# Kernel optimization log

Hardware: AMD Instinct MI355X
Metric: run time of the kernel (lower is better)

The kernel has to match this reference:

```python
import jax, jax.numpy as jnp
import numpy as np

GROUP_SIZE = 8
OUT_FEATURES = 4096
IN_FEATURES = 4096
G = OUT_FEATURES * IN_FEATURES // GROUP_SIZE  # number of quant groups


def setup_inputs() -> dict:
    key = jax.random.key(0)
    k1, k2, k3, k4, k5 = jax.random.split(key, 5)
    x = jax.random.normal(k1, (2, 2048, IN_FEATURES), dtype=jnp.float32)
    # packed uint8 bytes, stored as int32 for harness dtype support (values 0..255)
    weight_packed = jax.random.randint(k2, (G, GROUP_SIZE // 2), 0, 256, dtype=jnp.int32)
    weight_scale = jax.random.uniform(k3, (G, 1), dtype=jnp.float32)
    weight_bias = jax.random.normal(k4, (G, 1), dtype=jnp.float32)
    bias = jax.random.normal(k5, (OUT_FEATURES,), dtype=jnp.float32)
    return {"x": x, "weight_packed": weight_packed, "weight_scale": weight_scale,
            "weight_bias": weight_bias, "bias": bias}


def dequantize_4bit(packed, scale, wbias):
    # packed: [G, gs//2] ints in [0,256); each byte holds two 4-bit values
    low = (packed & 15).astype(jnp.float32)          # even positions
    high = ((packed >> 4) & 15).astype(jnp.float32)  # odd positions
    # interleave: q[:, ::2] = low, q[:, 1::2] = high
    q = jnp.stack([low, high], axis=-1).reshape(packed.shape[0], -1)  # [G, gs]
    return q * scale + wbias  # per-group scale and bias, broadcast [G,1]->[G,gs]


def reference(x, weight_packed, weight_scale, weight_bias, bias):
    w = dequantize_4bit(weight_packed, weight_scale, weight_bias)
    w = w.reshape(OUT_FEATURES, IN_FEATURES)
    # F.linear: y = x @ w.T + bias
    return jnp.einsum('bsi,oi->bso', x, w) + bias
```

## Files before the change

### kernel.cpp

```cpp
#include <hip/hip_runtime.h>
#include <hip/hip_bf16.h>
#include <stdint.h>

#define M_DIM 4096
#define N_DIM 4096
#define K_DIM 4096
#define NGROUPS (N_DIM * K_DIM / 8)

typedef __attribute__((ext_vector_type(4))) float f32x4;
typedef __attribute__((ext_vector_type(8))) short bf16x8;
typedef __attribute__((ext_vector_type(4))) int   i32x4;

__device__ __forceinline__ ushort f2bf(float f) {
  union { float f; uint32_t u; } v; v.f = f;
  uint32_t r = v.u + 0x7FFFu + ((v.u >> 16) & 1u);
  return (ushort)(r >> 16);
}

__global__ void k_dequant_w(const int* __restrict__ wp, const float* __restrict__ wsc,
                            const float* __restrict__ wbs, ushort* __restrict__ W) {
  const int g = blockIdx.x * 256 + threadIdx.x;
  i32x4 p = *(const i32x4*)(wp + (size_t)g * 4);
  const float s = wsc[g];
  const float b = wbs[g];
  bf16x8 o;
#pragma unroll
  for (int j = 0; j < 4; ++j) {
    const float lo = (float)(p[j] & 15)        * s + b;
    const float hi = (float)((p[j] >> 4) & 15) * s + b;
    o[2 * j]     = (short)f2bf(lo);
    o[2 * j + 1] = (short)f2bf(hi);
  }
  *(bf16x8*)(W + (size_t)g * 8) = o;
}

__global__ void k_cvt_x(const float* __restrict__ x, ushort* __restrict__ X) {
  const int t = blockIdx.x * 256 + threadIdx.x;
  f32x4 a = *(const f32x4*)(x + (size_t)t * 8);
  f32x4 b = *(const f32x4*)(x + (size_t)t * 8 + 4);
  bf16x8 o;
#pragma unroll
  for (int j = 0; j < 4; ++j) {
    o[j]     = (short)f2bf(a[j]);
    o[4 + j] = (short)f2bf(b[j]);
  }
  *(bf16x8*)(X + (size_t)t * 8) = o;
}


#define GLD(src, dst) __builtin_amdgcn_global_load_lds(                        \
    (const __attribute__((address_space(1))) void*)(src),                      \
    (__attribute__((address_space(3))) void*)(dst), 16, 0, 0)

__global__ __launch_bounds__(512, 2) void k_gemm_8ph(
    const ushort* __restrict__ A, const ushort* __restrict__ B,
    const float* __restrict__ bias, float* __restrict__ C) {
  __shared__ ushort sA[2][256 * 64];
  __shared__ ushort sB[2][256 * 64];
  const int tid  = threadIdx.x;
  const int lane = tid & 63;
  const int wid  = tid >> 6;
  const int wr   = wid >> 2;
  const int wc   = wid & 3;
  const int bm = blockIdx.x >> 4;
  const int bn = blockIdx.x & 15;

  const ushort* Ab = A + (size_t)bm * 256 * K_DIM;
  const ushort* Bb = B + (size_t)bn * 256 * K_DIM;

  const int srow = tid >> 3;
  const int scc  = (tid & 7) ^ ((tid >> 3) & 7);
  const int dofs = (tid >> 6) * 64 * 8;

  const int l15   = lane & 15;
  const int kx    = (lane >> 4) * 8;
  const int xsw   = (lane & 7) << 3;
  const int kidx0 = (0 * 32 + kx) ^ xsw;
  const int kidx1 = (1 * 32 + kx) ^ xsw;
  const int abase = (wr * 128 + l15) * 64;
  const int bbase = (wc * 64 + l15) * 64;

  f32x4 acc[8][4] = {};

#define STAGE_A(buf, kko)                                                      \
  _Pragma("unroll") for (int j = 0; j < 4; ++j)                                \
      GLD(Ab + (size_t)(j * 64 + srow) * K_DIM + (kko) + scc * 8,              \
          &sA[buf][j * 4096 + dofs]);
#define STAGE_B(buf, kko)                                                      \
  _Pragma("unroll") for (int j = 0; j < 4; ++j)                                \
      GLD(Bb + (size_t)(j * 64 + srow) * K_DIM + (kko) + scc * 8,              \
          &sB[buf][j * 4096 + dofs]);

  STAGE_A(0, 0);
  STAGE_B(0, 0);
  __syncthreads();

  bf16x8 af0[4][2], af1[4][2], bfA[2][2], bfB[2][2];
#pragma unroll
  for (int m = 0; m < 4; ++m) {
    af0[m][0] = *(const bf16x8*)(sA[0] + abase + m * 1024 + kidx0);
    af0[m][1] = *(const bf16x8*)(sA[0] + abase + m * 1024 + kidx1);
  }
#pragma unroll
  for (int n = 0; n < 2; ++n) {
    bfA[n][0] = *(const bf16x8*)(sB[0] + bbase + n * 1024 + kidx0);
    bfA[n][1] = *(const bf16x8*)(sB[0] + bbase + n * 1024 + kidx1);
  }

  for (int t = 0; t < 64; ++t) {
    const int b  = t & 1;
    const int kk = t * 64;
    const ushort* sAb = sA[b];
    const ushort* sBb = sB[b];
    const ushort* sAn = sA[b ^ 1];
    const ushort* sBn = sB[b ^ 1];

    if (t < 63) { STAGE_A(b ^ 1, kk + 64); }
#pragma unroll
    for (int n = 0; n < 2; ++n) {
      bfB[n][0] = *(const bf16x8*)(sBb + bbase + (2 + n) * 1024 + kidx0);
      bfB[n][1] = *(const bf16x8*)(sBb + bbase + (2 + n) * 1024 + kidx1);
    }
    __builtin_amdgcn_s_setprio(1);
#pragma unroll
    for (int m = 0; m < 4; ++m)
#pragma unroll
      for (int n = 0; n < 2; ++n)
#pragma unroll
        for (int kc = 0; kc < 2; ++kc)
          acc[m][n] = __builtin_amdgcn_mfma_f32_16x16x32_bf16(
              af0[m][kc], bfA[n][kc], acc[m][n], 0, 0, 0);
    __builtin_amdgcn_s_setprio(0);
    __builtin_amdgcn_s_barrier();

    if (t < 63) { STAGE_B(b ^ 1, kk + 64); }
#pragma unroll
    for (int m = 0; m < 4; ++m) {
      af1[m][0] = *(const bf16x8*)(sAb + abase + (4 + m) * 1024 + kidx0);
      af1[m][1] = *(const bf16x8*)(sAb + abase + (4 + m) * 1024 + kidx1);
    }
    __builtin_amdgcn_s_setprio(1);
#pragma unroll
    for (int m = 0; m < 4; ++m)
#pragma unroll
      for (int n = 0; n < 2; ++n)
#pragma unroll
        for (int kc = 0; kc < 2; ++kc)
          acc[m][2 + n] = __builtin_amdgcn_mfma_f32_16x16x32_bf16(
              af0[m][kc], bfB[n][kc], acc[m][2 + n], 0, 0, 0);
    __builtin_amdgcn_s_setprio(0);
    __builtin_amdgcn_s_barrier();

    __builtin_amdgcn_s_setprio(1);
#pragma unroll
    for (int m = 0; m < 4; ++m)
#pragma unroll
      for (int n = 0; n < 2; ++n)
#pragma unroll
        for (int kc = 0; kc < 2; ++kc)
          acc[4 + m][2 + n] = __builtin_amdgcn_mfma_f32_16x16x32_bf16(
              af1[m][kc], bfB[n][kc], acc[4 + m][2 + n], 0, 0, 0);
    __builtin_amdgcn_s_setprio(0);

    if (t < 63) { asm volatile("s_waitcnt vmcnt(0)" ::: "memory"); }
    __builtin_amdgcn_s_barrier();
    asm volatile("" ::: "memory");
    __builtin_amdgcn_s_setprio(1);
#pragma unroll
    for (int m = 0; m < 4; ++m)
#pragma unroll
      for (int n = 0; n < 2; ++n)
#pragma unroll
        for (int kc = 0; kc < 2; ++kc)
          acc[4 + m][n] = __builtin_amdgcn_mfma_f32_16x16x32_bf16(
              af1[m][kc], bfA[n][kc], acc[4 + m][n], 0, 0, 0);
    __builtin_amdgcn_s_setprio(0);
    if (t < 63) {
#pragma unroll
      for (int m = 0; m < 4; ++m) {
        af0[m][0] = *(const bf16x8*)(sAn + abase + m * 1024 + kidx0);
        af0[m][1] = *(const bf16x8*)(sAn + abase + m * 1024 + kidx1);
      }
#pragma unroll
      for (int n = 0; n < 2; ++n) {
        bfA[n][0] = *(const bf16x8*)(sBn + bbase + n * 1024 + kidx0);
        bfA[n][1] = *(const bf16x8*)(sBn + bbase + n * 1024 + kidx1);
      }
    }
  }

  const int fr = lane & 15;
  const int fq = lane >> 4;
  const int growbase = bm * 256 + wr * 128;
  const int gcolbase = bn * 256 + wc * 64;
#pragma unroll
  for (int ni = 0; ni < 4; ++ni) {
    const int col = gcolbase + ni * 16 + fr;
    const float bv = bias[col];
#pragma unroll
    for (int mi = 0; mi < 8; ++mi) {
      float* cp = C + (size_t)(growbase + mi * 16 + fq * 4) * N_DIM + col;
#pragma unroll
      for (int r = 0; r < 4; ++r)
        cp[(size_t)r * N_DIM] = acc[mi][ni][r] + bv;
    }
  }
}

__global__ void k_fallback(const float* __restrict__ x, const int* __restrict__ wp,
                           const float* __restrict__ wsc, const float* __restrict__ wbs,
                           const float* __restrict__ bias, float* __restrict__ y) {
  const int m = blockIdx.x;
  const int n = blockIdx.y * 256 + threadIdx.x;
  const float* xr = x + (size_t)m * K_DIM;
  const int gbase = n * (K_DIM / 8);
  float acc = 0.f;
  for (int g = 0; g < K_DIM / 8; ++g) {
    i32x4 p = *(const i32x4*)(wp + (size_t)(gbase + g) * 4);
    const float s = wsc[gbase + g];
    const float b = wbs[gbase + g];
    const float* xk = xr + g * 8;
#pragma unroll
    for (int j = 0; j < 4; ++j) {
      acc += ((float)(p[j] & 15)        * s + b) * xk[2 * j];
      acc += ((float)((p[j] >> 4) & 15) * s + b) * xk[2 * j + 1];
    }
  }
  y[(size_t)m * N_DIM + n] = acc + bias[n];
}

extern "C" void kernel_launch(void* const* d_in, const int* in_sizes, int n_in,
                              void* d_out, int out_size, void* d_ws, size_t ws_size,
                              hipStream_t stream) {
  const float* x    = (const float*)d_in[0];
  const int*   wp   = (const int*)d_in[1];
  const float* wsc  = (const float*)d_in[2];
  const float* wbs  = (const float*)d_in[3];
  const float* bias = (const float*)d_in[4];
  float* y = (float*)d_out;

  const size_t wbytes = (size_t)N_DIM * K_DIM * sizeof(ushort);
  const size_t xbytes = (size_t)M_DIM * K_DIM * sizeof(ushort);

  if (ws_size >= wbytes + xbytes) {
    ushort* Wbf = (ushort*)d_ws;
    ushort* Xbf = (ushort*)((char*)d_ws + wbytes);
    k_dequant_w<<<NGROUPS / 256, 256, 0, stream>>>(wp, wsc, wbs, Wbf);
    k_cvt_x<<<(M_DIM * K_DIM / 8) / 256, 256, 0, stream>>>(x, Xbf);
    k_gemm_8ph<<<16 * 16, 512, 0, stream>>>(Xbf, Wbf, bias, y);
  } else {
    k_fallback<<<dim3(M_DIM, N_DIM / 256), 256, 0, stream>>>(x, wp, wsc, wbs, bias, y);
  }
}
```

Before: 301.0 us.

## Restructure GEMM main loop with per-phase barriers and in-iteration fragment loads

The first A/B fragment loads move from the end of the previous iteration (the prefetch of the next buffer) to the start of the current iteration. Each of the four MFMA phases is now wrapped in sched_barrier plus s_barrier pairs, forcing the waves to proceed in lockstep with a fixed order of LDS reads, global-to-LDS staging and MFMA. This is meant to give the compiler and hardware a more predictable interleaving and avoid LDS or VMEM contention. In exchange it adds barriers and exposes the LDS fragment-load latency at the top of each iteration instead of hiding it behind the previous MFMAs.

```diff
diff --git a/kernel.cpp b/kernel.cpp
--- a/kernel.cpp
+++ b/kernel.cpp
@@ -96,61 +96,65 @@
   __syncthreads();
 
   bf16x8 af0[4][2], af1[4][2], bfA[2][2], bfB[2][2];
-#pragma unroll
-  for (int m = 0; m < 4; ++m) {
-    af0[m][0] = *(const bf16x8*)(sA[0] + abase + m * 1024 + kidx0);
-    af0[m][1] = *(const bf16x8*)(sA[0] + abase + m * 1024 + kidx1);
-  }
-#pragma unroll
-  for (int n = 0; n < 2; ++n) {
-    bfA[n][0] = *(const bf16x8*)(sB[0] + bbase + n * 1024 + kidx0);
-    bfA[n][1] = *(const bf16x8*)(sB[0] + bbase + n * 1024 + kidx1);
-  }
 
   for (int t = 0; t < 64; ++t) {
     const int b  = t & 1;
     const int kk = t * 64;
     const ushort* sAb = sA[b];
     const ushort* sBb = sB[b];
-    const ushort* sAn = sA[b ^ 1];
-    const ushort* sBn = sB[b ^ 1];
-
+
+#pragma unroll
+    for (int m = 0; m < 4; ++m) {
+      af0[m][0] = *(const bf16x8*)(sAb + abase + m * 1024 + kidx0);
+      af0[m][1] = *(const bf16x8*)(sAb + abase + m * 1024 + kidx1);
+    }
+#pragma unroll
+    for (int n = 0; n < 2; ++n) {
+      bfA[n][0] = *(const bf16x8*)(sBb + bbase + n * 1024 + kidx0);
+      bfA[n][1] = *(const bf16x8*)(sBb + bbase + n * 1024 + kidx1);
+    }
     if (t < 63) { STAGE_A(b ^ 1, kk + 64); }
+    __builtin_amdgcn_sched_barrier(0);
+    __builtin_amdgcn_s_barrier();
+    __builtin_amdgcn_s_setprio(1);
+#pragma unroll
+    for (int m = 0; m < 4; ++m)
+#pragma unroll
+      for (int n = 0; n < 2; ++n)
+#pragma unroll
+        for (int kc = 0; kc < 2; ++kc)
+          acc[m][n] = __builtin_amdgcn_mfma_f32_16x16x32_bf16(
+              af0[m][kc], bfA[n][kc], acc[m][n], 0, 0, 0);
+    __builtin_amdgcn_s_setprio(0);
+    __builtin_amdgcn_s_barrier();
+
 #pragma unroll
     for (int n = 0; n < 2; ++n) {
       bfB[n][0] = *(const bf16x8*)(sBb + bbase + (2 + n) * 1024 + kidx0);
       bfB[n][1] = *(const bf16x8*)(sBb + bbase + (2 + n) * 1024 + kidx1);
     }
-    __builtin_amdgcn_s_setprio(1);
-#pragma unroll
-    for (int m = 0; m < 4; ++m)
-#pragma unroll
-      for (int n = 0; n < 2; ++n)
-#pragma unroll
-        for (int kc = 0; kc < 2; ++kc)
-          acc[m][n] = __builtin_amdgcn_mfma_f32_16x16x32_bf16(
-              af0[m][kc], bfA[n][kc], acc[m][n], 0, 0, 0);
-    __builtin_amdgcn_s_setprio(0);
-    __builtin_amdgcn_s_barrier();
-
     if (t < 63) { STAGE_B(b ^ 1, kk + 64); }
+    __builtin_amdgcn_sched_barrier(0);
+    __builtin_amdgcn_s_barrier();
+    __builtin_amdgcn_s_setprio(1);
+#pragma unroll
+    for (int m = 0; m < 4; ++m)
+#pragma unroll
+      for (int n = 0; n < 2; ++n)
+#pragma unroll
+        for (int kc = 0; kc < 2; ++kc)
+          acc[m][2 + n] = __builtin_amdgcn_mfma_f32_16x16x32_bf16(
+              af0[m][kc], bfB[n][kc], acc[m][2 + n], 0, 0, 0);
+    __builtin_amdgcn_s_setprio(0);
+    __builtin_amdgcn_s_barrier();
+
 #pragma unroll
     for (int m = 0; m < 4; ++m) {
       af1[m][0] = *(const bf16x8*)(sAb + abase + (4 + m) * 1024 + kidx0);
       af1[m][1] = *(const bf16x8*)(sAb + abase + (4 + m) * 1024 + kidx1);
     }
-    __builtin_amdgcn_s_setprio(1);
-#pragma unroll
-    for (int m = 0; m < 4; ++m)
-#pragma unroll
-      for (int n = 0; n < 2; ++n)
-#pragma unroll
-        for (int kc = 0; kc < 2; ++kc)
-          acc[m][2 + n] = __builtin_amdgcn_mfma_f32_16x16x32_bf16(
-              af0[m][kc], bfB[n][kc], acc[m][2 + n], 0, 0, 0);
-    __builtin_amdgcn_s_setprio(0);
-    __builtin_amdgcn_s_barrier();
-
+    __builtin_amdgcn_sched_barrier(0);
+    __builtin_amdgcn_s_barrier();
     __builtin_amdgcn_s_setprio(1);
 #pragma unroll
     for (int m = 0; m < 4; ++m)
@@ -161,10 +165,10 @@
           acc[4 + m][2 + n] = __builtin_amdgcn_mfma_f32_16x16x32_bf16(
               af1[m][kc], bfB[n][kc], acc[4 + m][2 + n], 0, 0, 0);
     __builtin_amdgcn_s_setprio(0);
+    __builtin_amdgcn_s_barrier();
 
     if (t < 63) { asm volatile("s_waitcnt vmcnt(0)" ::: "memory"); }
     __builtin_amdgcn_s_barrier();
-    asm volatile("" ::: "memory");
     __builtin_amdgcn_s_setprio(1);
 #pragma unroll
     for (int m = 0; m < 4; ++m)
@@ -175,18 +179,7 @@
           acc[4 + m][n] = __builtin_amdgcn_mfma_f32_16x16x32_bf16(
               af1[m][kc], bfA[n][kc], acc[4 + m][n], 0, 0, 0);
     __builtin_amdgcn_s_setprio(0);
-    if (t < 63) {
-#pragma unroll
-      for (int m = 0; m < 4; ++m) {
-        af0[m][0] = *(const bf16x8*)(sAn + abase + m * 1024 + kidx0);
-        af0[m][1] = *(const bf16x8*)(sAn + abase + m * 1024 + kidx1);
-      }
-#pragma unroll
-      for (int n = 0; n < 2; ++n) {
-        bfA[n][0] = *(const bf16x8*)(sBn + bbase + n * 1024 + kidx0);
-        bfA[n][1] = *(const bf16x8*)(sBn + bbase + n * 1024 + kidx1);
-      }
-    }
+    __builtin_amdgcn_s_barrier();
   }
 
   const int fr = lane & 15;
```

Result: no change. 297.0 us (-1.3%).
